# Kernel tuning notes

Measured on AMD Instinct MI355X. Metric: run time of the kernel, lower is better.

## Reference

```python
import jax, jax.numpy as jnp
import numpy as np

B = 512      # batch
T = 16       # tokens per instruction
V = 1000     # vocab
E = 4        # num_experts
K = 1        # active experts per layer
NLAYERS = 3
TOPK_LOGIC = 32


def _conv(x, w, b, stride=2):
    # x: [B,Cin,H,W], w: [Cout,Cin,3,3] (OIHW), padding=1, stride=2
    y = jax.lax.conv_general_dilated(
        x, w, window_strides=(stride, stride), padding=((1, 1), (1, 1)),
        dimension_numbers=('NCHW', 'OIHW', 'NCHW'))
    return y + b[None, :, None, None]


def _gated_conv(x, w, b, gate):
    # w: [E,Cout,Cin,3,3], b: [E,Cout], gate: [B,E] 0/1 mask
    # Faithful to original: all experts computed densely, then masked.
    outs = jax.vmap(lambda wi, bi: _conv(x, wi, bi))(w, b)  # [E,B,Cout,H',W']
    return jnp.einsum('ebchw,be->bchw', outs, gate)


def _topk_mask(logits, k):
    # 0/1 mask with ones at the top-k positions along the last axis
    _, idx = jax.lax.top_k(logits, k)
    return jnp.sum(jax.nn.one_hot(idx, logits.shape[-1], dtype=logits.dtype), axis=-2)


def setup_inputs() -> dict:
    key = jax.random.key(0)
    ks = jax.random.split(key, 16)
    def rn(k, shape, s=0.05):
        return jax.random.normal(k, shape, jnp.float32) * s
    return dict(
        img=jax.random.normal(ks[0], (B, 12, 56, 56), jnp.float32),
        text=jax.random.randint(ks[1], (B, T), 0, V),
        prev_action=jax.random.randint(ks[2], (B,), 0, 7),
        emb_table=rn(ks[3], (V, 32), 1.0),
        r_w1=rn(ks[4], (32, 64)), r_b1=jnp.zeros((64,), jnp.float32),
        r_w2=rn(ks[5], (64, NLAYERS * E)), r_b2=jnp.zeros((NLAYERS * E,), jnp.float32),
        l_w1=rn(ks[6], (32, 64)), l_b1=jnp.zeros((64,), jnp.float32),
        l_w2=rn(ks[7], (64, 256)), l_b2=jnp.zeros((256,), jnp.float32),
        c1_w=rn(ks[8], (E, 32, 12, 3, 3)), c1_b=jnp.zeros((E, 32), jnp.float32),
        c2_w=rn(ks[9], (E, 64, 32, 3, 3)), c2_b=jnp.zeros((E, 64), jnp.float32),
        c3_w=rn(ks[10], (E, 128, 64, 3, 3)), c3_b=jnp.zeros((E, 128), jnp.float32),
        act_emb=rn(ks[11], (7, 16), 1.0),
        f_w=rn(ks[12], (6272 + 32 + 16, 256)), f_b=jnp.zeros((256,), jnp.float32),
        h_w=rn(ks[13], (256, 5)), h_b=jnp.zeros((5,), jnp.float32),
    )


def reference(img, text, prev_action, emb_table, r_w1, r_b1, r_w2, r_b2,
              l_w1, l_b1, l_w2, l_b2, c1_w, c1_b, c2_w, c2_b, c3_w, c3_b,
              act_emb, f_w, f_b, h_w, h_b):
    # EmbeddingBag(mode='mean') over token dim
    lang = jnp.mean(emb_table[text], axis=1)                      # [B,32]
    # Router: MLP -> [B,3,E] logits, top-k scatter -> 0/1 mask
    rlog = (jax.nn.relu(lang @ r_w1 + r_b1) @ r_w2 + r_b2).reshape(-1, NLAYERS, E)
    masks = _topk_mask(rlog, K)                                   # [B,3,E]
    x = jax.nn.relu(_gated_conv(img, c1_w, c1_b, masks[:, 0, :])) # [B,32,28,28]
    x = jax.nn.relu(_gated_conv(x, c2_w, c2_b, masks[:, 1, :]))   # [B,64,14,14]
    x = jax.nn.relu(_gated_conv(x, c3_w, c3_b, masks[:, 2, :]))   # [B,128,7,7]
    vis = x.reshape(x.shape[0], -1)                               # [B,6272]
    act = act_emb[prev_action]                                    # [B,16]
    fused = jnp.concatenate([vis, lang, act], axis=1)             # [B,6320]
    hidden = fused @ f_w + f_b                                    # [B,256]
    logic = jax.nn.relu(lang @ l_w1 + l_b1) @ l_w2 + l_b2         # [B,256]
    lmask = _topk_mask(logic, TOPK_LOGIC)                         # [B,256]
    out = jax.nn.relu(hidden * lmask)                             # dropout is identity in eval
    logits = out @ h_w + h_b                                      # [B,5]
    return logits, rlog
```

## Files before the change

### kernel.cpp

```cpp
#include <hip/hip_runtime.h>
#include <hip/hip_bf16.h>


typedef __bf16 bf16x8 __attribute__((ext_vector_type(8)));
typedef float f32x4 __attribute__((ext_vector_type(4)));

__device__ __forceinline__ unsigned short f2bf(float f) {
  union { float f; unsigned u; } v; v.f = f;
  unsigned r = v.u + 0x7FFFu + ((v.u >> 16) & 1u);
  return (unsigned short)(r >> 16);
}

__device__ __forceinline__ int wswz(int b) { return b ^ (((b >> 7) & 3) << 4); }

__global__ __launch_bounds__(256) void prep_kernel(
    const int* __restrict__ text, const float* __restrict__ emb,
    const float* __restrict__ r_w1, const float* __restrict__ r_b1,
    const float* __restrict__ r_w2, const float* __restrict__ r_b2,
    const float* __restrict__ l_w1, const float* __restrict__ l_b1,
    const float* __restrict__ l_w2, const float* __restrict__ l_b2,
    const float* __restrict__ act_emb, const int* __restrict__ pa,
    const float* __restrict__ c1_w, const float* __restrict__ c2_w,
    const float* __restrict__ c3_w, const float* __restrict__ fw,
    float* __restrict__ rlog_out, int* __restrict__ eidx, float* __restrict__ lmask,
    unsigned short* __restrict__ tailb,
    unsigned short* __restrict__ wb1, unsigned short* __restrict__ wb2,
    unsigned short* __restrict__ wb3, unsigned short* __restrict__ fwT) {
  __shared__ __align__(16) unsigned short tl2[64][272];
  const int blk = blockIdx.x;
  const int tid = threadIdx.x;

  if (blk < 512) {
    int b = blk;
    int t = tid;
    __shared__ float lg[32];
    __shared__ float hr[64];
    __shared__ float hl[64];
    __shared__ float rl[12];
    __shared__ float lgc[256];

    if (t < 32) {
      const int* tb = text + b * 16;
      float s = 0.f;
#pragma unroll
      for (int tok = 0; tok < 16; ++tok) s += emb[tb[tok] * 32 + t];
      lg[t] = s * 0.0625f;
    }
    __syncthreads();

    if (t < 64) {
      float s1 = r_b1[t], s2 = l_b1[t];
      for (int k = 0; k < 32; ++k) {
        float lv = lg[k];
        s1 += lv * r_w1[k * 64 + t];
        s2 += lv * l_w1[k * 64 + t];
      }
      hr[t] = fmaxf(s1, 0.f);
      hl[t] = fmaxf(s2, 0.f);
    }
    if (t < 64) {
      float v = 0.f;
      if (t < 32) v = lg[t];
      else if (t < 48) v = act_emb[pa[b] * 16 + (t - 32)];
      tailb[b * 64 + t] = f2bf(v);
    }
    __syncthreads();

    if (t < 12) {
      float s = r_b2[t];
      for (int k = 0; k < 64; ++k) s += hr[k] * r_w2[k * 12 + t];
      rl[t] = s;
      rlog_out[b * 12 + t] = s;
    }
    {
      float s = l_b2[t];
      for (int k = 0; k < 64; ++k) s += hl[k] * l_w2[k * 256 + t];
      lgc[t] = s;
    }
    __syncthreads();

    if (t < 3) {
      int best = 0;
      float bv = rl[t * 4];
      for (int e = 1; e < 4; ++e) {
        float v = rl[t * 4 + e];
        if (v > bv) { bv = v; best = e; }
      }
      eidx[b * 3 + t] = best;
    }
    {
      float v = lgc[t];
      int cnt = 0;
      for (int k = 0; k < 256; ++k) {
        float u = lgc[k];
        cnt += (u > v) || (u == v && k < t);
      }
      lmask[b * 256 + t] = (cnt < 32) ? 1.f : 0.f;
    }
  } else if (blk < 2080) {
    int idx = (blk - 512) * 256 + tid;
    if (idx < 24576) {
      int k = idx % 192, ec = idx / 192;
      float v = 0.f;
      if (k < 144) {
        int g = k >> 4, ci = k & 15;
        if (ci < 12) v = c1_w[ec * 108 + ci * 9 + g];
      }
      wb1[idx] = f2bf(v);
    } else if (idx < 106496) {
      int i2 = idx - 24576;
      int k = i2 % 320, ec = i2 / 320;
      float v = 0.f;
      if (k < 288) {
        int g = k >> 5, ci = k & 31;
        v = c2_w[ec * 288 + ci * 9 + g];
      }
      wb2[i2] = f2bf(v);
    } else {
      int i3 = idx - 106496;
      int k = i3 % 576, ec = i3 / 576;
      int g = k >> 6, ci = k & 63;
      wb3[i3] = f2bf(c3_w[ec * 576 + ci * 9 + g]);
    }
  } else {
    int kb = blk - 2080;
    int k0 = kb * 64;
#pragma unroll
    for (int rg = 0; rg < 4; ++rg) {
      int rl = rg * 16 + (tid >> 4);
      int srow;
      bool valid;
      if (kb < 98) {
        srow = ((kb & 1) * 64 + rl) * 49 + (kb >> 1);
        valid = true;
      } else {
        srow = 6272 + rl;
        valid = (rl < 48);
      }
#pragma unroll
      for (int c = 0; c < 4; ++c) {
        int col = ((tid & 15) + c * 16) * 4;
        float4 v = valid ? *(const float4*)&fw[(size_t)srow * 256 + col]
                         : (float4){0.f, 0.f, 0.f, 0.f};
        tl2[rl][col + 0] = f2bf(v.x);
        tl2[rl][col + 1] = f2bf(v.y);
        tl2[rl][col + 2] = f2bf(v.z);
        tl2[rl][col + 3] = f2bf(v.w);
      }
    }
    __syncthreads();
#pragma unroll
    for (int np = 0; np < 4; ++np) {
      int n = np * 64 + (tid >> 2);
      int kc = (tid & 3) * 16;
      unsigned short vv[16];
#pragma unroll
      for (int i = 0; i < 16; ++i) vv[i] = tl2[kc + i][n];
      unsigned short* dst = fwT + (size_t)n * 6336 + k0 + kc;
      *(uint4*)dst = *(const uint4*)&vv[0];
      *(uint4*)(dst + 8) = *(const uint4*)&vv[8];
    }
  }
}

__global__ __launch_bounds__(256) void conv1_fused(
    const float* __restrict__ img, const unsigned short* __restrict__ wb,
    const float* __restrict__ bias, const int* __restrict__ eidx,
    unsigned short* __restrict__ out, int* __restrict__ cnt,
    int* __restrict__ perm) {
  __shared__ __align__(16) char win[25536];
  __shared__ __align__(16) char ldsB[3 * 4096];
  const int tid = threadIdx.x;

  if (blockIdx.x >= 3584) {
    int* el = (int*)win;
    int* cc = el + 512;
    int l = blockIdx.x - 3584;
    el[tid] = eidx[tid * 3 + l];
    el[tid + 256] = eidx[(tid + 256) * 3 + l];
    __syncthreads();
    if (tid < 4) {
      int c = 0;
      for (int b = 0; b < 512; ++b) c += (el[b] == tid);
      cc[tid] = c;
      cnt[l * 4 + tid] = c;
    }
    __syncthreads();
#pragma unroll
    for (int rep = 0; rep < 2; ++rep) {
      int b = tid + rep * 256;
      int e = el[b];
      int rank = 0;
      for (int bp = 0; bp < b; ++bp) rank += (el[bp] == e);
      int off = 0;
      for (int ee = 0; ee < e; ++ee) off += cc[ee];
      perm[l * 512 + off + rank] = b;
    }
    return;
  }

  const int xcd = blockIdx.x & 7;
  const int u = blockIdx.x >> 3;
  const int t = u % 7;
  const int s = (u / 7) * 8 + xcd;
  const int e = eidx[s * 3];
  const int lane = tid & 63;
  const int wid = tid >> 6;
  const int wm0 = wid * 32;

  const int p0 = t * 128;
  const int ohmin = p0 / 28;
  const int ih0 = ohmin * 2 - 1;

  const float* ibase = img + (size_t)s * 37632;
  float vv[9][4];
  int bp9[9];
  bool ok9[9];
#pragma unroll
  for (int it = 0; it < 9; ++it) {
    int c = tid + it * 256;
    int q = c / 728;
    int rem = c - q * 728;
    int ihl = rem / 56;
    int iw = rem - ihl * 56;
    int ih = ih0 + ihl;
    bool ok = (c < 2184) && ((unsigned)ih < 56u);
    ok9[it] = ok;
    bp9[it] = (ihl * 57 + iw + 1) * 32 + q * 8;
    if (ok) {
      const float* src = ibase + q * 12544 + ih * 56 + iw;
      vv[it][0] = src[0];
      vv[it][1] = src[3136];
      vv[it][2] = src[6272];
      vv[it][3] = src[9408];
    }
  }
  uint4 bstg[3];
  int bdst[3];
  {
    const unsigned short* wbe = wb + e * (32 * 192);
#pragma unroll
    for (int c = 0; c < 3; ++c) {
      int cc = tid + 256 * c;
      int n = cc / 24, cb = cc - n * 24;
      int kt = cb >> 3, cbl = cb & 7;
      bstg[c] = *(const uint4*)(wbe + n * 192 + cb * 8);
      bdst[c] = kt * 4096 + n * 128 + ((cbl * 16) ^ ((n & 7) << 4));
    }
  }
  __builtin_amdgcn_sched_barrier(0);

  {
    uint4 z; z.x = z.y = z.z = z.w = 0u;
    for (int i = tid; i < 1596; i += 256) ((uint4*)win)[i] = z;
  }
#pragma unroll
  for (int c = 0; c < 3; ++c) *(uint4*)(ldsB + bdst[c]) = bstg[c];
  __syncthreads();

#pragma unroll
  for (int it = 0; it < 9; ++it) {
    if (ok9[it]) {
      unsigned short w4[4] = {f2bf(vv[it][0]), f2bf(vv[it][1]),
                              f2bf(vv[it][2]), f2bf(vv[it][3])};
      *(unsigned long long*)(win + wswz(bp9[it])) = *(const unsigned long long*)w4;
    }
  }

  int ohl[2], owr[2];
#pragma unroll
  for (int mf = 0; mf < 2; ++mf) {
    int m = wm0 + mf * 16 + (lane & 15);
    int p = p0 + m;
    if (p > 783) p = 783;
    int oh = p / 28;
    owr[mf] = p - oh * 28;
    ohl[mf] = (oh - ohmin) * 2;
  }
  const int lg = lane >> 4;
  const int ci0 = (lg & 1) * 8;
  const int lgh = lg >> 1;
  int brdo[2], brx[2];
#pragma unroll
  for (int nf = 0; nf < 2; ++nf) {
    int n = nf * 16 + (lane & 15);
    brdo[nf] = n * 128;
    brx[nf] = (n & 7) << 4;
  }

  f32x4 acc[2][2];
#pragma unroll
  for (int mf = 0; mf < 2; ++mf)
#pragma unroll
    for (int nf = 0; nf < 2; ++nf) acc[mf][nf] = (f32x4){0.f, 0.f, 0.f, 0.f};

  __syncthreads();

#pragma unroll
  for (int kt = 0; kt < 3; ++kt) {
#pragma unroll
    for (int ks = 0; ks < 2; ++ks) {
      const int g = kt * 4 + ks * 2 + lgh;
      const int kh = g / 3;
      const int kw = g - kh * 3;
      const bool gv = (g < 9);
      bf16x8 af[2];
#pragma unroll
      for (int mf = 0; mf < 2; ++mf) {
        int iwp = owr[mf] * 2 + kw;
        int ihl = ohl[mf] + kh;
        int bp = gv ? ((ihl * 57 + iwp) * 32 + ci0 * 2)
                    : (13 * 57 * 32 + ci0 * 2);
        af[mf] = __builtin_bit_cast(bf16x8, *(const uint4*)(win + wswz(bp)));
      }
      bf16x8 bfv[2];
      const int cb = ks * 64 + ((lane >> 4) << 4);
#pragma unroll
      for (int nf = 0; nf < 2; ++nf)
        bfv[nf] = __builtin_bit_cast(bf16x8,
            *(const uint4*)(ldsB + kt * 4096 + brdo[nf] + (cb ^ brx[nf])));
#pragma unroll
      for (int mf = 0; mf < 2; ++mf)
#pragma unroll
        for (int nf = 0; nf < 2; ++nf)
          acc[mf][nf] = __builtin_amdgcn_mfma_f32_16x16x32_bf16(af[mf], bfv[nf], acc[mf][nf], 0, 0, 0);
    }
  }

  const int col = lane & 15;
  const int rg = (lane >> 4) * 4;
  const float b0 = bias[e * 32 + col];
  const float b1 = bias[e * 32 + 16 + col];
#pragma unroll
  for (int mf = 0; mf < 2; ++mf)
#pragma unroll
    for (int r = 0; r < 4; ++r) {
      int m = wm0 + mf * 16 + rg + r;
      int p = p0 + m;
      if (p < 784) {
        size_t ob = ((size_t)s * 784 + p) * 32;
        out[ob + col]      = f2bf(fmaxf(acc[mf][0][r] + b0, 0.f));
        out[ob + 16 + col] = f2bf(fmaxf(acc[mf][1][r] + b1, 0.f));
      }
    }
}

template<int CIN, int H, int OH, int KREAL, int KP, int COUT,
         int WGM, int WGN, int MF, int NF>
__global__ __launch_bounds__(256) void conv_mfma(
    const unsigned short* __restrict__ in, const unsigned short* __restrict__ wb,
    const float* __restrict__ bias, const int* __restrict__ cnt,
    const int* __restrict__ perm, unsigned short* __restrict__ out) {
  constexpr int PerS = OH * OH;
  constexpr int BM = WGM * MF * 16;
  constexpr int BN = WGN * NF * 16;
  constexpr int AJ = BM / 32;
  constexpr int KT = KP / 64;
  constexpr int W = H;
  constexpr int BCH = BN / 32;

  int bm = blockIdx.x;
  int e = 0, row0 = 0, rows = 0;
  bool found = false;
  {
    int acc = 0, ebase = 0;
#pragma unroll
    for (int ee = 0; ee < 4; ++ee) {
      int er = cnt[ee] * PerS;
      int te = (er + BM - 1) / BM;
      if (!found && bm < acc + te) {
        e = ee;
        row0 = ebase + (bm - acc) * BM;
        rows = er - (bm - acc) * BM;
        if (rows > BM) rows = BM;
        found = true;
      }
      acc += te;
      ebase += er;
    }
  }
  if (!found) return;

  __shared__ __align__(16) char lds[BM * 128 + BN * 128];
  char* ldsB = lds + BM * 128;
  const int tid = threadIdx.x;
  const int lane = tid & 63;
  const int wid = tid >> 6;
  const int wm0 = (wid / WGN) * (MF * 16);
  const int wn0 = (wid % WGN) * (NF * 16);
  const int c16 = tid & 7;

  int ihc[AJ], iwc[AJ], abase[AJ], adso[AJ];
#pragma unroll
  for (int j = 0; j < AJ; ++j) {
    int r = (tid >> 3) + 32 * j;
    int gr = row0 + r;
    const int MAXR = 512 * PerS - 1;
    if (gr > MAXR) gr = MAXR;
    int sord = gr / PerS;
    int p = gr - sord * PerS;
    int s = perm[sord];
    int oh = p / OH, ow = p - oh * OH;
    ihc[j] = oh * 2 - 1;
    iwc[j] = ow * 2 - 1;
    abase[j] = s * (H * W);
    adso[j] = r * 128 + ((c16 * 16) ^ ((r & 7) << 4));
  }
  const unsigned short* wbe = wb + (size_t)e * COUT * KP;
  int bgo[BCH], bdso[BCH];
#pragma unroll
  for (int c = 0; c < BCH; ++c) {
    int cc = tid + 256 * c;
    int n = cc >> 3, cb = cc & 7;
    bgo[c] = n * KP + cb * 8;
    bdso[c] = n * 128 + ((cb * 16) ^ ((n & 7) << 4));
  }
  int ardo[MF], arx[MF], brdo[NF], brx[NF];
#pragma unroll
  for (int mf = 0; mf < MF; ++mf) {
    int r = wm0 + mf * 16 + (lane & 15);
    ardo[mf] = r * 128;
    arx[mf] = (r & 7) << 4;
  }
#pragma unroll
  for (int nf = 0; nf < NF; ++nf) {
    int n = wn0 + nf * 16 + (lane & 15);
    brdo[nf] = n * 128;
    brx[nf] = (n & 7) << 4;
  }

  auto loadA = [&](int kt, int j) -> uint4 {
    uint4 z; z.x = z.y = z.z = z.w = 0u;
    int kbase = kt * 64 + c16 * 8;
    if (kbase >= KREAL) return z;
    int g = kbase / CIN;
    int ci0 = kbase - g * CIN;
    int kh = g / 3, kw = g - (g / 3) * 3;
    int ih = ihc[j] + kh, iw = iwc[j] + kw;
    if ((unsigned)ih >= (unsigned)H || (unsigned)iw >= (unsigned)W) return z;
    const unsigned short* p = in + ((size_t)(abase[j] + ih * W + iw) * CIN + ci0);
    return *(const uint4*)p;
  };

  uint4 rA[AJ], rB[BCH];
#pragma unroll
  for (int j = 0; j < AJ; ++j) rA[j] = loadA(0, j);
#pragma unroll
  for (int c = 0; c < BCH; ++c) rB[c] = *(const uint4*)(wbe + bgo[c]);

  f32x4 acc[MF][NF];
#pragma unroll
  for (int mf = 0; mf < MF; ++mf)
#pragma unroll
    for (int nf = 0; nf < NF; ++nf) acc[mf][nf] = (f32x4){0.f, 0.f, 0.f, 0.f};

  for (int kt = 0; kt < KT; ++kt) {
    __syncthreads();
#pragma unroll
    for (int j = 0; j < AJ; ++j) *(uint4*)(lds + adso[j]) = rA[j];
#pragma unroll
    for (int c = 0; c < BCH; ++c) *(uint4*)(ldsB + bdso[c]) = rB[c];
    __syncthreads();
    if (kt + 1 < KT) {
#pragma unroll
      for (int j = 0; j < AJ; ++j) rA[j] = loadA(kt + 1, j);
#pragma unroll
      for (int c = 0; c < BCH; ++c) rB[c] = *(const uint4*)(wbe + bgo[c] + (kt + 1) * 64);
    }
#pragma unroll
    for (int ks = 0; ks < 2; ++ks) {
      int cb = ks * 64 + ((lane >> 4) << 4);
      bf16x8 af[MF], bfv[NF];
#pragma unroll
      for (int mf = 0; mf < MF; ++mf)
        af[mf] = __builtin_bit_cast(bf16x8, *(const uint4*)(lds + ardo[mf] + (cb ^ arx[mf])));
#pragma unroll
      for (int nf = 0; nf < NF; ++nf)
        bfv[nf] = __builtin_bit_cast(bf16x8, *(const uint4*)(ldsB + brdo[nf] + (cb ^ brx[nf])));
#pragma unroll
      for (int mf = 0; mf < MF; ++mf)
#pragma unroll
        for (int nf = 0; nf < NF; ++nf)
          acc[mf][nf] = __builtin_amdgcn_mfma_f32_16x16x32_bf16(af[mf], bfv[nf], acc[mf][nf], 0, 0, 0);
    }
  }

  const int col = lane & 15;
  const int rg = (lane >> 4) * 4;
#pragma unroll
  for (int mf = 0; mf < MF; ++mf) {
#pragma unroll
    for (int r = 0; r < 4; ++r) {
      int m = wm0 + mf * 16 + rg + r;
      if (m < rows) {
        int gr = row0 + m;
        int sord = gr / PerS;
        int p = gr - sord * PerS;
        int s = perm[sord];
        size_t ob = ((size_t)s * PerS + p) * COUT;
#pragma unroll
        for (int nf = 0; nf < NF; ++nf) {
          int co = wn0 + nf * 16 + col;
          float v = acc[mf][nf][r] + bias[e * COUT + co];
          out[ob + co] = f2bf(fmaxf(v, 0.f));
        }
      }
    }
  }
}

__global__ __launch_bounds__(256) void fgemm_kernel(
    const unsigned short* __restrict__ x3, const unsigned short* __restrict__ tail,
    const unsigned short* __restrict__ fwT, float* __restrict__ partial) {
  constexpr int MF = 2, NF = 2;
  const int row0 = blockIdx.x * 64;
  const int nc0 = blockIdx.y * 64;
  const int kz = blockIdx.z * 704;
  __shared__ __align__(16) char lds[64 * 128 + 64 * 128];
  char* ldsB = lds + 64 * 128;
  const int tid = threadIdx.x;
  const int lane = tid & 63;
  const int wid = tid >> 6;
  const int wm0 = (wid >> 1) * 32;
  const int wn0 = (wid & 1) * 32;
  const int c16 = tid & 7;
  int arow[2], adso[2];
#pragma unroll
  for (int j = 0; j < 2; ++j) {
    int r = (tid >> 3) + 32 * j;
    arow[j] = row0 + r;
    adso[j] = r * 128 + ((c16 * 16) ^ ((r & 7) << 4));
  }
  int bgo[2], bdso[2];
#pragma unroll
  for (int c = 0; c < 2; ++c) {
    int cc = tid + 256 * c;
    int n = cc >> 3, cb = cc & 7;
    bgo[c] = (nc0 + n) * 6336 + kz + cb * 8;
    bdso[c] = n * 128 + ((cb * 16) ^ ((n & 7) << 4));
  }
  int ardo[MF], arx[MF], brdo[NF], brx[NF];
#pragma unroll
  for (int mf = 0; mf < MF; ++mf) {
    int r = wm0 + mf * 16 + (lane & 15);
    ardo[mf] = r * 128; arx[mf] = (r & 7) << 4;
  }
#pragma unroll
  for (int nf = 0; nf < NF; ++nf) {
    int n = wn0 + nf * 16 + (lane & 15);
    brdo[nf] = n * 128; brx[nf] = (n & 7) << 4;
  }
  auto loadA = [&](int kt, int j) -> uint4 {
    int k = kz + kt * 64 + c16 * 8;
    const unsigned short* p;
    if (k < 6272) p = x3 + (size_t)arow[j] * 6272 + k;
    else p = tail + arow[j] * 64 + (k - 6272);
    return *(const uint4*)p;
  };
  uint4 rA[2], rB[2];
#pragma unroll
  for (int j = 0; j < 2; ++j) rA[j] = loadA(0, j);
#pragma unroll
  for (int c = 0; c < 2; ++c) rB[c] = *(const uint4*)(fwT + bgo[c]);
  f32x4 acc[MF][NF];
#pragma unroll
  for (int mf = 0; mf < MF; ++mf)
#pragma unroll
    for (int nf = 0; nf < NF; ++nf) acc[mf][nf] = (f32x4){0.f, 0.f, 0.f, 0.f};

  for (int kt = 0; kt < 11; ++kt) {
    __syncthreads();
#pragma unroll
    for (int j = 0; j < 2; ++j) *(uint4*)(lds + adso[j]) = rA[j];
#pragma unroll
    for (int c = 0; c < 2; ++c) *(uint4*)(ldsB + bdso[c]) = rB[c];
    __syncthreads();
    if (kt + 1 < 11) {
#pragma unroll
      for (int j = 0; j < 2; ++j) rA[j] = loadA(kt + 1, j);
#pragma unroll
      for (int c = 0; c < 2; ++c) rB[c] = *(const uint4*)(fwT + bgo[c] + (kt + 1) * 64);
    }
#pragma unroll
    for (int ks = 0; ks < 2; ++ks) {
      int cb = ks * 64 + ((lane >> 4) << 4);
      bf16x8 af[MF], bfv[NF];
#pragma unroll
      for (int mf = 0; mf < MF; ++mf)
        af[mf] = __builtin_bit_cast(bf16x8, *(const uint4*)(lds + ardo[mf] + (cb ^ arx[mf])));
#pragma unroll
      for (int nf = 0; nf < NF; ++nf)
        bfv[nf] = __builtin_bit_cast(bf16x8, *(const uint4*)(ldsB + brdo[nf] + (cb ^ brx[nf])));
#pragma unroll
      for (int mf = 0; mf < MF; ++mf)
#pragma unroll
        for (int nf = 0; nf < NF; ++nf)
          acc[mf][nf] = __builtin_amdgcn_mfma_f32_16x16x32_bf16(af[mf], bfv[nf], acc[mf][nf], 0, 0, 0);
    }
  }
  const int col = lane & 15;
  const int rg = (lane >> 4) * 4;
  float* pz = partial + (size_t)blockIdx.z * 131072;
#pragma unroll
  for (int mf = 0; mf < MF; ++mf)
#pragma unroll
    for (int r = 0; r < 4; ++r) {
      int m = wm0 + mf * 16 + rg + r;
      int grow = row0 + m;
#pragma unroll
      for (int nf = 0; nf < 2; ++nf) {
        int n = nc0 + wn0 + nf * 16 + col;
        pz[grow * 256 + n] = acc[mf][nf][r];
      }
    }
}

__global__ __launch_bounds__(256) void reduce_head(const float* __restrict__ part,
                                                   const float* __restrict__ f_b,
                                                   const float* __restrict__ lmask,
                                                   const float* __restrict__ h_w,
                                                   const float* __restrict__ h_b,
                                                   float* __restrict__ logits) {
  int b = blockIdx.x, t = threadIdx.x;
  float s = f_b[t];
#pragma unroll
  for (int z = 0; z < 9; ++z) s += part[z * 131072 + b * 256 + t];
  __shared__ float o[256];
  o[t] = (lmask[b * 256 + t] != 0.f) ? fmaxf(s, 0.f) : 0.f;
  __syncthreads();
  if (t < 5) {
    float v = h_b[t];
    for (int n = 0; n < 256; ++n) v += o[n] * h_w[n * 5 + t];
    logits[b * 5 + t] = v;
  }
}

extern "C" void kernel_launch(void* const* d_in, const int* in_sizes, int n_in,
                              void* d_out, int out_size, void* d_ws, size_t ws_size,
                              hipStream_t stream) {
  (void)in_sizes; (void)n_in; (void)out_size; (void)ws_size;
  const float* img       = (const float*)d_in[0];
  const int*   text      = (const int*)d_in[1];
  const int*   pa        = (const int*)d_in[2];
  const float* emb_table = (const float*)d_in[3];
  const float* r_w1 = (const float*)d_in[4];
  const float* r_b1 = (const float*)d_in[5];
  const float* r_w2 = (const float*)d_in[6];
  const float* r_b2 = (const float*)d_in[7];
  const float* l_w1 = (const float*)d_in[8];
  const float* l_b1 = (const float*)d_in[9];
  const float* l_w2 = (const float*)d_in[10];
  const float* l_b2 = (const float*)d_in[11];
  const float* c1_w = (const float*)d_in[12];
  const float* c1_b = (const float*)d_in[13];
  const float* c2_w = (const float*)d_in[14];
  const float* c2_b = (const float*)d_in[15];
  const float* c3_w = (const float*)d_in[16];
  const float* c3_b = (const float*)d_in[17];
  const float* act_emb = (const float*)d_in[18];
  const float* f_w = (const float*)d_in[19];
  const float* f_b = (const float*)d_in[20];
  const float* h_w = (const float*)d_in[21];
  const float* h_b = (const float*)d_in[22];

  float* outf   = (float*)d_out;
  float* logits = outf;
  float* rlog   = outf + 2560;

  char* cur = (char*)d_ws;
  auto alloc = [&](size_t bytes) { char* r = cur; cur += (bytes + 255) & ~(size_t)255; return r; };
  float* lmask   = (float*)alloc(131072 * 4);
  int* eidx      = (int*)alloc(1536 * 4);
  int* cnt       = (int*)alloc(12 * 4);
  int* perm      = (int*)alloc(1536 * 4);
  unsigned short* wb1  = (unsigned short*)alloc((size_t)24576 * 2);
  unsigned short* wb2  = (unsigned short*)alloc((size_t)81920 * 2);
  unsigned short* wb3  = (unsigned short*)alloc((size_t)294912 * 2);
  unsigned short* fwT  = (unsigned short*)alloc((size_t)1622016 * 2);
  unsigned short* tailb= (unsigned short*)alloc((size_t)32768 * 2);
  unsigned short* x1b  = (unsigned short*)alloc((size_t)12845056 * 2);
  unsigned short* x2b  = (unsigned short*)alloc((size_t)6422528 * 2);
  unsigned short* x3b  = (unsigned short*)alloc((size_t)3211264 * 2);
  float* partial       = (float*)alloc((size_t)9 * 131072 * 4);

  prep_kernel<<<2179, 256, 0, stream>>>(text, emb_table,
                                        r_w1, r_b1, r_w2, r_b2,
                                        l_w1, l_b1, l_w2, l_b2,
                                        act_emb, pa,
                                        c1_w, c2_w, c3_w, f_w,
                                        rlog, eidx, lmask, tailb,
                                        wb1, wb2, wb3, fwT);

  conv1_fused<<<3587, 256, 0, stream>>>(img, wb1, c1_b, eidx, x1b, cnt, perm);
  conv_mfma<32, 28, 14, 288, 320, 64, 2, 2, 4, 2>
      <<<787, 256, 0, stream>>>(x1b, wb2, c2_b, cnt + 4, perm + 512, x2b);
  conv_mfma<64, 14, 7, 576, 576, 128, 1, 4, 4, 2>
      <<<395, 256, 0, stream>>>(x2b, wb3, c3_b, cnt + 8, perm + 1024, x3b);

  fgemm_kernel<<<dim3(8, 4, 9), 256, 0, stream>>>(x3b, tailb, fwT, partial);
  reduce_head<<<512, 256, 0, stream>>>(partial, f_b, lmask, h_w, h_b, logits);
}
```

Baseline: 138.3 us.

## Fuse prep and conv1 into one kernel with per-block router recompute

Merges the prep kernel and the conv1 kernel into a single launch. Each conv1 block recomputes its sample's layer-0 router expert from the text embedding and converts its expert's conv1 weights to bf16 in place, instead of reading precomputed eidx and wb1. The three perm blocks recompute the router for all samples on their own. This removes one kernel launch and the serial dependency between them, at the cost of redundant router MLP and weight-conversion work in every conv1 block plus heavier per-thread router loops in the perm blocks.

```diff
diff --git a/kernel.cpp b/kernel.cpp
--- a/kernel.cpp
+++ b/kernel.cpp
@@ -13,7 +13,8 @@
 
 __device__ __forceinline__ int wswz(int b) { return b ^ (((b >> 7) & 3) << 4); }
 
-__global__ __launch_bounds__(256) void prep_kernel(
+__global__ __launch_bounds__(256) void megaA(
+    const float* __restrict__ img,
     const int* __restrict__ text, const float* __restrict__ emb,
     const float* __restrict__ r_w1, const float* __restrict__ r_b1,
     const float* __restrict__ r_w2, const float* __restrict__ r_b2,
@@ -22,22 +23,265 @@
     const float* __restrict__ act_emb, const int* __restrict__ pa,
     const float* __restrict__ c1_w, const float* __restrict__ c2_w,
     const float* __restrict__ c3_w, const float* __restrict__ fw,
-    float* __restrict__ rlog_out, int* __restrict__ eidx, float* __restrict__ lmask,
+    const float* __restrict__ c1_b,
+    float* __restrict__ rlog_out, float* __restrict__ lmask,
     unsigned short* __restrict__ tailb,
-    unsigned short* __restrict__ wb1, unsigned short* __restrict__ wb2,
-    unsigned short* __restrict__ wb3, unsigned short* __restrict__ fwT) {
-  __shared__ __align__(16) unsigned short tl2[64][272];
+    unsigned short* __restrict__ wb2, unsigned short* __restrict__ wb3,
+    unsigned short* __restrict__ fwT,
+    unsigned short* __restrict__ x1b,
+    int* __restrict__ cnt, int* __restrict__ perm) {
+  __shared__ __align__(16) char shm[38400];
+  const int tid = threadIdx.x;
   const int blk = blockIdx.x;
-  const int tid = threadIdx.x;
-
-  if (blk < 512) {
-    int b = blk;
+
+  if (blk < 3584) {
+    char* win  = shm;
+    char* ldsB = shm + 25536;
+    float* shLang = (float*)(shm + 37888);
+    float* shHr   = shLang + 32;
+    float* shRl   = shHr + 64;
+
+    const int xcd = blk & 7;
+    const int u = blk >> 3;
+    const int t = u % 7;
+    const int s = (u / 7) * 8 + xcd;
+    const int lane = tid & 63;
+    const int wid = tid >> 6;
+    const int wm0 = wid * 32;
+
+    const int p0 = t * 128;
+    const int ohmin = p0 / 28;
+    const int ih0 = ohmin * 2 - 1;
+
+    const float* ibase = img + (size_t)s * 37632;
+    float vv[9][4];
+    int bp9[9];
+    bool ok9[9];
+#pragma unroll
+    for (int it = 0; it < 9; ++it) {
+      int c = tid + it * 256;
+      int q = c / 728;
+      int rem = c - q * 728;
+      int ihl = rem / 56;
+      int iw = rem - ihl * 56;
+      int ih = ih0 + ihl;
+      bool ok = (c < 2184) && ((unsigned)ih < 56u);
+      ok9[it] = ok;
+      bp9[it] = (ihl * 57 + iw + 1) * 32 + q * 8;
+      if (ok) {
+        const float* src = ibase + q * 12544 + ih * 56 + iw;
+        vv[it][0] = src[0];
+        vv[it][1] = src[3136];
+        vv[it][2] = src[6272];
+        vv[it][3] = src[9408];
+      }
+    }
+    __builtin_amdgcn_sched_barrier(0);
+
+    if (tid < 32) {
+      const int* tb = text + s * 16;
+      float acc = 0.f;
+#pragma unroll
+      for (int tok = 0; tok < 16; ++tok) acc += emb[tb[tok] * 32 + tid];
+      shLang[tid] = acc * 0.0625f;
+    }
+    __syncthreads();
+    if (tid < 64) {
+      float s1 = r_b1[tid];
+      for (int k = 0; k < 32; ++k) s1 += shLang[k] * r_w1[k * 64 + tid];
+      shHr[tid] = fmaxf(s1, 0.f);
+    }
+    __syncthreads();
+    if (tid < 4) {
+      float v = r_b2[tid];
+      for (int k = 0; k < 64; ++k) v += shHr[k] * r_w2[k * 12 + tid];
+      shRl[tid] = v;
+    }
+    __syncthreads();
+    int e;
+    {
+      float r0 = shRl[0], r1 = shRl[1], r2 = shRl[2], r3 = shRl[3];
+      int best = 0; float bv = r0;
+      if (r1 > bv) { bv = r1; best = 1; }
+      if (r2 > bv) { bv = r2; best = 2; }
+      if (r3 > bv) { bv = r3; best = 3; }
+      e = best;
+    }
+
+    unsigned short w8s[3][8];
+    int bdst[3];
+    {
+      const float* c1e = c1_w + e * 3456;
+#pragma unroll
+      for (int c = 0; c < 3; ++c) {
+        int cc = tid + 256 * c;
+        int n = cc / 24, cb = cc - n * 24;
+#pragma unroll
+        for (int j = 0; j < 8; ++j) {
+          int k = cb * 8 + j;
+          int g = k >> 4, ci = k & 15;
+          float v = (g < 9 && ci < 12) ? c1e[n * 108 + ci * 9 + g] : 0.f;
+          w8s[c][j] = f2bf(v);
+        }
+        int kt = cb >> 3, cbl = cb & 7;
+        bdst[c] = kt * 4096 + n * 128 + ((cbl * 16) ^ ((n & 7) << 4));
+      }
+    }
+    {
+      uint4 z; z.x = z.y = z.z = z.w = 0u;
+      for (int i = tid; i < 1596; i += 256) ((uint4*)win)[i] = z;
+    }
+#pragma unroll
+    for (int c = 0; c < 3; ++c) *(uint4*)(ldsB + bdst[c]) = *(const uint4*)w8s[c];
+    __syncthreads();
+
+#pragma unroll
+    for (int it = 0; it < 9; ++it) {
+      if (ok9[it]) {
+        unsigned short w4[4] = {f2bf(vv[it][0]), f2bf(vv[it][1]),
+                                f2bf(vv[it][2]), f2bf(vv[it][3])};
+        *(unsigned long long*)(win + wswz(bp9[it])) = *(const unsigned long long*)w4;
+      }
+    }
+
+    int ohl[2], owr[2];
+#pragma unroll
+    for (int mf = 0; mf < 2; ++mf) {
+      int m = wm0 + mf * 16 + (lane & 15);
+      int p = p0 + m;
+      if (p > 783) p = 783;
+      int oh = p / 28;
+      owr[mf] = p - oh * 28;
+      ohl[mf] = (oh - ohmin) * 2;
+    }
+    const int lg = lane >> 4;
+    const int ci0 = (lg & 1) * 8;
+    const int lgh = lg >> 1;
+    int brdo[2], brx[2];
+#pragma unroll
+    for (int nf = 0; nf < 2; ++nf) {
+      int n = nf * 16 + (lane & 15);
+      brdo[nf] = n * 128;
+      brx[nf] = (n & 7) << 4;
+    }
+
+    f32x4 acc[2][2];
+#pragma unroll
+    for (int mf = 0; mf < 2; ++mf)
+#pragma unroll
+      for (int nf = 0; nf < 2; ++nf) acc[mf][nf] = (f32x4){0.f, 0.f, 0.f, 0.f};
+
+    __syncthreads();
+
+#pragma unroll
+    for (int kt = 0; kt < 3; ++kt) {
+#pragma unroll
+      for (int ks = 0; ks < 2; ++ks) {
+        const int g = kt * 4 + ks * 2 + lgh;
+        const int kh = g / 3;
+        const int kw = g - kh * 3;
+        const bool gv = (g < 9);
+        bf16x8 af[2];
+#pragma unroll
+        for (int mf = 0; mf < 2; ++mf) {
+          int iwp = owr[mf] * 2 + kw;
+          int ihl = ohl[mf] + kh;
+          int bp = gv ? ((ihl * 57 + iwp) * 32 + ci0 * 2)
+                      : (13 * 57 * 32 + ci0 * 2);
+          af[mf] = __builtin_bit_cast(bf16x8, *(const uint4*)(win + wswz(bp)));
+        }
+        bf16x8 bfv[2];
+        const int cb = ks * 64 + ((lane >> 4) << 4);
+#pragma unroll
+        for (int nf = 0; nf < 2; ++nf)
+          bfv[nf] = __builtin_bit_cast(bf16x8,
+              *(const uint4*)(ldsB + kt * 4096 + brdo[nf] + (cb ^ brx[nf])));
+#pragma unroll
+        for (int mf = 0; mf < 2; ++mf)
+#pragma unroll
+          for (int nf = 0; nf < 2; ++nf)
+            acc[mf][nf] = __builtin_amdgcn_mfma_f32_16x16x32_bf16(af[mf], bfv[nf], acc[mf][nf], 0, 0, 0);
+      }
+    }
+
+    const int col = lane & 15;
+    const int rg = (lane >> 4) * 4;
+    const float b0 = c1_b[e * 32 + col];
+    const float b1 = c1_b[e * 32 + 16 + col];
+#pragma unroll
+    for (int mf = 0; mf < 2; ++mf)
+#pragma unroll
+      for (int r = 0; r < 4; ++r) {
+        int m = wm0 + mf * 16 + rg + r;
+        int p = p0 + m;
+        if (p < 784) {
+          size_t ob = ((size_t)s * 784 + p) * 32;
+          x1b[ob + col]      = f2bf(fmaxf(acc[mf][0][r] + b0, 0.f));
+          x1b[ob + 16 + col] = f2bf(fmaxf(acc[mf][1][r] + b1, 0.f));
+        }
+      }
+  } else if (blk < 3587) {
+    int* el = (int*)shm;
+    int* ccx = el + 512;
+    int l = blk - 3584;
+#pragma unroll
+    for (int rep = 0; rep < 2; ++rep) {
+      int b = tid + rep * 256;
+      const int* tb = text + b * 16;
+      float lang[32];
+#pragma unroll
+      for (int d = 0; d < 32; ++d) lang[d] = 0.f;
+#pragma unroll
+      for (int tok = 0; tok < 16; ++tok) {
+        int row = tb[tok] * 32;
+#pragma unroll
+        for (int d = 0; d < 32; ++d) lang[d] += emb[row + d];
+      }
+#pragma unroll
+      for (int d = 0; d < 32; ++d) lang[d] *= 0.0625f;
+      float rl4[4];
+#pragma unroll
+      for (int tt = 0; tt < 4; ++tt) rl4[tt] = r_b2[l * 4 + tt];
+#pragma unroll 2
+      for (int k = 0; k < 64; ++k) {
+        float hk = r_b1[k];
+#pragma unroll
+        for (int j = 0; j < 32; ++j) hk += lang[j] * r_w1[j * 64 + k];
+        hk = fmaxf(hk, 0.f);
+#pragma unroll
+        for (int tt = 0; tt < 4; ++tt) rl4[tt] += hk * r_w2[k * 12 + l * 4 + tt];
+      }
+      int best = 0; float bv = rl4[0];
+#pragma unroll
+      for (int ee = 1; ee < 4; ++ee) { if (rl4[ee] > bv) { bv = rl4[ee]; best = ee; } }
+      el[b] = best;
+    }
+    __syncthreads();
+    if (tid < 4) {
+      int c = 0;
+      for (int b = 0; b < 512; ++b) c += (el[b] == tid);
+      ccx[tid] = c;
+      cnt[l * 4 + tid] = c;
+    }
+    __syncthreads();
+#pragma unroll
+    for (int rep = 0; rep < 2; ++rep) {
+      int b = tid + rep * 256;
+      int e = el[b];
+      int rank = 0;
+      for (int bp = 0; bp < b; ++bp) rank += (el[bp] == e);
+      int off = 0;
+      for (int ee = 0; ee < e; ++ee) off += ccx[ee];
+      perm[l * 512 + off + rank] = b;
+    }
+  } else if (blk < 4099) {
+    int b = blk - 3587;
     int t = tid;
-    __shared__ float lg[32];
-    __shared__ float hr[64];
-    __shared__ float hl[64];
-    __shared__ float rl[12];
-    __shared__ float lgc[256];
+    float* lg   = (float*)shm;
+    float* hr   = lg + 32;
+    float* hl   = hr + 64;
+    float* rl   = hl + 64;
+    float* lgc  = rl + 12;
 
     if (t < 32) {
       const int* tb = text + b * 16;
@@ -79,51 +323,34 @@
     }
     __syncthreads();
 
-    if (t < 3) {
-      int best = 0;
-      float bv = rl[t * 4];
-      for (int e = 1; e < 4; ++e) {
-        float v = rl[t * 4 + e];
-        if (v > bv) { bv = v; best = e; }
-      }
-      eidx[b * 3 + t] = best;
-    }
     {
       float v = lgc[t];
-      int cnt = 0;
+      int cnt2 = 0;
       for (int k = 0; k < 256; ++k) {
-        float u = lgc[k];
-        cnt += (u > v) || (u == v && k < t);
-      }
-      lmask[b * 256 + t] = (cnt < 32) ? 1.f : 0.f;
-    }
-  } else if (blk < 2080) {
-    int idx = (blk - 512) * 256 + tid;
-    if (idx < 24576) {
-      int k = idx % 192, ec = idx / 192;
-      float v = 0.f;
-      if (k < 144) {
-        int g = k >> 4, ci = k & 15;
-        if (ci < 12) v = c1_w[ec * 108 + ci * 9 + g];
-      }
-      wb1[idx] = f2bf(v);
-    } else if (idx < 106496) {
-      int i2 = idx - 24576;
-      int k = i2 % 320, ec = i2 / 320;
+        float u2 = lgc[k];
+        cnt2 += (u2 > v) || (u2 == v && k < t);
+      }
+      lmask[b * 256 + t] = (cnt2 < 32) ? 1.f : 0.f;
+    }
+  } else if (blk < 5571) {
+    int idx = (blk - 4099) * 256 + tid;
+    if (idx < 81920) {
+      int k = idx % 320, ec = idx / 320;
       float v = 0.f;
       if (k < 288) {
         int g = k >> 5, ci = k & 31;
         v = c2_w[ec * 288 + ci * 9 + g];
       }
-      wb2[i2] = f2bf(v);
+      wb2[idx] = f2bf(v);
     } else {
-      int i3 = idx - 106496;
+      int i3 = idx - 81920;
       int k = i3 % 576, ec = i3 / 576;
       int g = k >> 6, ci = k & 63;
       wb3[i3] = f2bf(c3_w[ec * 576 + ci * 9 + g]);
     }
   } else {
-    int kb = blk - 2080;
+    unsigned short(*tl2)[272] = (unsigned short(*)[272])shm;
+    int kb = blk - 5571;
     int k0 = kb * 64;
 #pragma unroll
     for (int rg = 0; rg < 4; ++rg) {
@@ -153,196 +380,14 @@
     for (int np = 0; np < 4; ++np) {
       int n = np * 64 + (tid >> 2);
       int kc = (tid & 3) * 16;
-      unsigned short vv[16];
-#pragma unroll
-      for (int i = 0; i < 16; ++i) vv[i] = tl2[kc + i][n];
+      unsigned short vv2[16];
+#pragma unroll
+      for (int i = 0; i < 16; ++i) vv2[i] = tl2[kc + i][n];
       unsigned short* dst = fwT + (size_t)n * 6336 + k0 + kc;
-      *(uint4*)dst = *(const uint4*)&vv[0];
-      *(uint4*)(dst + 8) = *(const uint4*)&vv[8];
-    }
-  }
-}
-
-__global__ __launch_bounds__(256) void conv1_fused(
-    const float* __restrict__ img, const unsigned short* __restrict__ wb,
-    const float* __restrict__ bias, const int* __restrict__ eidx,
-    unsigned short* __restrict__ out, int* __restrict__ cnt,
-    int* __restrict__ perm) {
-  __shared__ __align__(16) char win[25536];
-  __shared__ __align__(16) char ldsB[3 * 4096];
-  const int tid = threadIdx.x;
-
-  if (blockIdx.x >= 3584) {
-    int* el = (int*)win;
-    int* cc = el + 512;
-    int l = blockIdx.x - 3584;
-    el[tid] = eidx[tid * 3 + l];
-    el[tid + 256] = eidx[(tid + 256) * 3 + l];
-    __syncthreads();
-    if (tid < 4) {
-      int c = 0;
-      for (int b = 0; b < 512; ++b) c += (el[b] == tid);
-      cc[tid] = c;
-      cnt[l * 4 + tid] = c;
-    }
-    __syncthreads();
-#pragma unroll
-    for (int rep = 0; rep < 2; ++rep) {
-      int b = tid + rep * 256;
-      int e = el[b];
-      int rank = 0;
-      for (int bp = 0; bp < b; ++bp) rank += (el[bp] == e);
-      int off = 0;
-      for (int ee = 0; ee < e; ++ee) off += cc[ee];
-      perm[l * 512 + off + rank] = b;
-    }
-    return;
-  }
-
-  const int xcd = blockIdx.x & 7;
-  const int u = blockIdx.x >> 3;
-  const int t = u % 7;
-  const int s = (u / 7) * 8 + xcd;
-  const int e = eidx[s * 3];
-  const int lane = tid & 63;
-  const int wid = tid >> 6;
-  const int wm0 = wid * 32;
-
-  const int p0 = t * 128;
-  const int ohmin = p0 / 28;
-  const int ih0 = ohmin * 2 - 1;
-
-  const float* ibase = img + (size_t)s * 37632;
-  float vv[9][4];
-  int bp9[9];
-  bool ok9[9];
-#pragma unroll
-  for (int it = 0; it < 9; ++it) {
-    int c = tid + it * 256;
-    int q = c / 728;
-    int rem = c - q * 728;
-    int ihl = rem / 56;
-    int iw = rem - ihl * 56;
-    int ih = ih0 + ihl;
-    bool ok = (c < 2184) && ((unsigned)ih < 56u);
-    ok9[it] = ok;
-    bp9[it] = (ihl * 57 + iw + 1) * 32 + q * 8;
-    if (ok) {
-      const float* src = ibase + q * 12544 + ih * 56 + iw;
-      vv[it][0] = src[0];
-      vv[it][1] = src[3136];
-      vv[it][2] = src[6272];
-      vv[it][3] = src[9408];
-    }
-  }
-  uint4 bstg[3];
-  int bdst[3];
-  {
-    const unsigned short* wbe = wb + e * (32 * 192);
-#pragma unroll
-    for (int c = 0; c < 3; ++c) {
-      int cc = tid + 256 * c;
-      int n = cc / 24, cb = cc - n * 24;
-      int kt = cb >> 3, cbl = cb & 7;
-      bstg[c] = *(const uint4*)(wbe + n * 192 + cb * 8);
-      bdst[c] = kt * 4096 + n * 128 + ((cbl * 16) ^ ((n & 7) << 4));
-    }
-  }
-  __builtin_amdgcn_sched_barrier(0);
-
-  {
-    uint4 z; z.x = z.y = z.z = z.w = 0u;
-    for (int i = tid; i < 1596; i += 256) ((uint4*)win)[i] = z;
-  }
-#pragma unroll
-  for (int c = 0; c < 3; ++c) *(uint4*)(ldsB + bdst[c]) = bstg[c];
-  __syncthreads();
-
-#pragma unroll
-  for (int it = 0; it < 9; ++it) {
-    if (ok9[it]) {
-      unsigned short w4[4] = {f2bf(vv[it][0]), f2bf(vv[it][1]),
-                              f2bf(vv[it][2]), f2bf(vv[it][3])};
-      *(unsigned long long*)(win + wswz(bp9[it])) = *(const unsigned long long*)w4;
-    }
-  }
-
-  int ohl[2], owr[2];
-#pragma unroll
-  for (int mf = 0; mf < 2; ++mf) {
-    int m = wm0 + mf * 16 + (lane & 15);
-    int p = p0 + m;
-    if (p > 783) p = 783;
-    int oh = p / 28;
-    owr[mf] = p - oh * 28;
-    ohl[mf] = (oh - ohmin) * 2;
-  }
-  const int lg = lane >> 4;
-  const int ci0 = (lg & 1) * 8;
-  const int lgh = lg >> 1;
-  int brdo[2], brx[2];
-#pragma unroll
-  for (int nf = 0; nf < 2; ++nf) {
-    int n = nf * 16 + (lane & 15);
-    brdo[nf] = n * 128;
-    brx[nf] = (n & 7) << 4;
-  }
-
-  f32x4 acc[2][2];
-#pragma unroll
-  for (int mf = 0; mf < 2; ++mf)
-#pragma unroll
-    for (int nf = 0; nf < 2; ++nf) acc[mf][nf] = (f32x4){0.f, 0.f, 0.f, 0.f};
-
-  __syncthreads();
-
-#pragma unroll
-  for (int kt = 0; kt < 3; ++kt) {
-#pragma unroll
-    for (int ks = 0; ks < 2; ++ks) {
-      const int g = kt * 4 + ks * 2 + lgh;
-      const int kh = g / 3;
-      const int kw = g - kh * 3;
-      const bool gv = (g < 9);
-      bf16x8 af[2];
-#pragma unroll
-      for (int mf = 0; mf < 2; ++mf) {
-        int iwp = owr[mf] * 2 + kw;
-        int ihl = ohl[mf] + kh;
-        int bp = gv ? ((ihl * 57 + iwp) * 32 + ci0 * 2)
-                    : (13 * 57 * 32 + ci0 * 2);
-        af[mf] = __builtin_bit_cast(bf16x8, *(const uint4*)(win + wswz(bp)));
-      }
-      bf16x8 bfv[2];
-      const int cb = ks * 64 + ((lane >> 4) << 4);
-#pragma unroll
-      for (int nf = 0; nf < 2; ++nf)
-        bfv[nf] = __builtin_bit_cast(bf16x8,
-            *(const uint4*)(ldsB + kt * 4096 + brdo[nf] + (cb ^ brx[nf])));
-#pragma unroll
-      for (int mf = 0; mf < 2; ++mf)
-#pragma unroll
-        for (int nf = 0; nf < 2; ++nf)
-          acc[mf][nf] = __builtin_amdgcn_mfma_f32_16x16x32_bf16(af[mf], bfv[nf], acc[mf][nf], 0, 0, 0);
-    }
-  }
-
-  const int col = lane & 15;
-  const int rg = (lane >> 4) * 4;
-  const float b0 = bias[e * 32 + col];
-  const float b1 = bias[e * 32 + 16 + col];
-#pragma unroll
-  for (int mf = 0; mf < 2; ++mf)
-#pragma unroll
-    for (int r = 0; r < 4; ++r) {
-      int m = wm0 + mf * 16 + rg + r;
-      int p = p0 + m;
-      if (p < 784) {
-        size_t ob = ((size_t)s * 784 + p) * 32;
-        out[ob + col]      = f2bf(fmaxf(acc[mf][0][r] + b0, 0.f));
-        out[ob + 16 + col] = f2bf(fmaxf(acc[mf][1][r] + b1, 0.f));
-      }
-    }
+      *(uint4*)dst = *(const uint4*)&vv2[0];
+      *(uint4*)(dst + 8) = *(const uint4*)&vv2[8];
+    }
+  }
 }
 
 template<int CIN, int H, int OH, int KREAL, int KP, int COUT,
@@ -670,10 +715,8 @@
   char* cur = (char*)d_ws;
   auto alloc = [&](size_t bytes) { char* r = cur; cur += (bytes + 255) & ~(size_t)255; return r; };
   float* lmask   = (float*)alloc(131072 * 4);
-  int* eidx      = (int*)alloc(1536 * 4);
   int* cnt       = (int*)alloc(12 * 4);
   int* perm      = (int*)alloc(1536 * 4);
-  unsigned short* wb1  = (unsigned short*)alloc((size_t)24576 * 2);
   unsigned short* wb2  = (unsigned short*)alloc((size_t)81920 * 2);
   unsigned short* wb3  = (unsigned short*)alloc((size_t)294912 * 2);
   unsigned short* fwT  = (unsigned short*)alloc((size_t)1622016 * 2);
@@ -683,15 +726,14 @@
   unsigned short* x3b  = (unsigned short*)alloc((size_t)3211264 * 2);
   float* partial       = (float*)alloc((size_t)9 * 131072 * 4);
 
-  prep_kernel<<<2179, 256, 0, stream>>>(text, emb_table,
-                                        r_w1, r_b1, r_w2, r_b2,
-                                        l_w1, l_b1, l_w2, l_b2,
-                                        act_emb, pa,
-                                        c1_w, c2_w, c3_w, f_w,
-                                        rlog, eidx, lmask, tailb,
-                                        wb1, wb2, wb3, fwT);
-
-  conv1_fused<<<3587, 256, 0, stream>>>(img, wb1, c1_b, eidx, x1b, cnt, perm);
+  megaA<<<5670, 256, 0, stream>>>(img, text, emb_table,
+                                  r_w1, r_b1, r_w2, r_b2,
+                                  l_w1, l_b1, l_w2, l_b2,
+                                  act_emb, pa,
+                                  c1_w, c2_w, c3_w, f_w, c1_b,
+                                  rlog, lmask, tailb,
+                                  wb2, wb3, fwT, x1b, cnt, perm);
+
   conv_mfma<32, 28, 14, 288, 320, 64, 2, 2, 4, 2>
       <<<787, 256, 0, stream>>>(x1b, wb2, c2_b, cnt + 4, perm + 512, x2b);
   conv_mfma<64, 14, 7, 576, 576, 128, 1, 4, 4, 2>
```

Measured after the change: 212.9 us. 1.54x slower.

## Move weight conversion into conv1 kernel and build conv1 weights inline

Applied to the files above, without the earlier changes.

The conv2/conv3 weight bf16 repacking and the fc weight transpose move out of the prep kernel into extra blocks of the conv1 kernel, so they run alongside conv1 instead of lengthening the serial prep stage. Conv1 blocks now read fp32 c1 weights directly and convert them to bf16 in registers, which removes the intermediate wb1 buffer and its dependency on prep. The cost is more scalar global loads per conv1 block and a larger combined shared-memory footprint.

```diff
diff --git a/kernel.cpp b/kernel.cpp
--- a/kernel.cpp
+++ b/kernel.cpp
@@ -20,157 +20,150 @@
     const float* __restrict__ l_w1, const float* __restrict__ l_b1,
     const float* __restrict__ l_w2, const float* __restrict__ l_b2,
     const float* __restrict__ act_emb, const int* __restrict__ pa,
-    const float* __restrict__ c1_w, const float* __restrict__ c2_w,
-    const float* __restrict__ c3_w, const float* __restrict__ fw,
     float* __restrict__ rlog_out, int* __restrict__ eidx, float* __restrict__ lmask,
-    unsigned short* __restrict__ tailb,
-    unsigned short* __restrict__ wb1, unsigned short* __restrict__ wb2,
-    unsigned short* __restrict__ wb3, unsigned short* __restrict__ fwT) {
-  __shared__ __align__(16) unsigned short tl2[64][272];
-  const int blk = blockIdx.x;
-  const int tid = threadIdx.x;
-
-  if (blk < 512) {
-    int b = blk;
-    int t = tid;
-    __shared__ float lg[32];
-    __shared__ float hr[64];
-    __shared__ float hl[64];
-    __shared__ float rl[12];
-    __shared__ float lgc[256];
-
-    if (t < 32) {
-      const int* tb = text + b * 16;
-      float s = 0.f;
-#pragma unroll
-      for (int tok = 0; tok < 16; ++tok) s += emb[tb[tok] * 32 + t];
-      lg[t] = s * 0.0625f;
-    }
-    __syncthreads();
-
-    if (t < 64) {
-      float s1 = r_b1[t], s2 = l_b1[t];
-      for (int k = 0; k < 32; ++k) {
-        float lv = lg[k];
-        s1 += lv * r_w1[k * 64 + t];
-        s2 += lv * l_w1[k * 64 + t];
-      }
-      hr[t] = fmaxf(s1, 0.f);
-      hl[t] = fmaxf(s2, 0.f);
-    }
-    if (t < 64) {
-      float v = 0.f;
-      if (t < 32) v = lg[t];
-      else if (t < 48) v = act_emb[pa[b] * 16 + (t - 32)];
-      tailb[b * 64 + t] = f2bf(v);
-    }
-    __syncthreads();
-
-    if (t < 12) {
-      float s = r_b2[t];
-      for (int k = 0; k < 64; ++k) s += hr[k] * r_w2[k * 12 + t];
-      rl[t] = s;
-      rlog_out[b * 12 + t] = s;
-    }
-    {
-      float s = l_b2[t];
-      for (int k = 0; k < 64; ++k) s += hl[k] * l_w2[k * 256 + t];
-      lgc[t] = s;
-    }
-    __syncthreads();
-
-    if (t < 3) {
-      int best = 0;
-      float bv = rl[t * 4];
-      for (int e = 1; e < 4; ++e) {
-        float v = rl[t * 4 + e];
-        if (v > bv) { bv = v; best = e; }
-      }
-      eidx[b * 3 + t] = best;
-    }
-    {
-      float v = lgc[t];
-      int cnt = 0;
-      for (int k = 0; k < 256; ++k) {
-        float u = lgc[k];
-        cnt += (u > v) || (u == v && k < t);
-      }
-      lmask[b * 256 + t] = (cnt < 32) ? 1.f : 0.f;
-    }
-  } else if (blk < 2080) {
-    int idx = (blk - 512) * 256 + tid;
-    if (idx < 24576) {
-      int k = idx % 192, ec = idx / 192;
-      float v = 0.f;
-      if (k < 144) {
-        int g = k >> 4, ci = k & 15;
-        if (ci < 12) v = c1_w[ec * 108 + ci * 9 + g];
-      }
-      wb1[idx] = f2bf(v);
-    } else if (idx < 106496) {
-      int i2 = idx - 24576;
-      int k = i2 % 320, ec = i2 / 320;
-      float v = 0.f;
-      if (k < 288) {
-        int g = k >> 5, ci = k & 31;
-        v = c2_w[ec * 288 + ci * 9 + g];
-      }
-      wb2[i2] = f2bf(v);
-    } else {
-      int i3 = idx - 106496;
-      int k = i3 % 576, ec = i3 / 576;
-      int g = k >> 6, ci = k & 63;
-      wb3[i3] = f2bf(c3_w[ec * 576 + ci * 9 + g]);
-    }
-  } else {
-    int kb = blk - 2080;
-    int k0 = kb * 64;
-#pragma unroll
-    for (int rg = 0; rg < 4; ++rg) {
-      int rl = rg * 16 + (tid >> 4);
-      int srow;
-      bool valid;
-      if (kb < 98) {
-        srow = ((kb & 1) * 64 + rl) * 49 + (kb >> 1);
-        valid = true;
-      } else {
-        srow = 6272 + rl;
-        valid = (rl < 48);
-      }
-#pragma unroll
-      for (int c = 0; c < 4; ++c) {
-        int col = ((tid & 15) + c * 16) * 4;
-        float4 v = valid ? *(const float4*)&fw[(size_t)srow * 256 + col]
-                         : (float4){0.f, 0.f, 0.f, 0.f};
-        tl2[rl][col + 0] = f2bf(v.x);
-        tl2[rl][col + 1] = f2bf(v.y);
-        tl2[rl][col + 2] = f2bf(v.z);
-        tl2[rl][col + 3] = f2bf(v.w);
-      }
-    }
-    __syncthreads();
-#pragma unroll
-    for (int np = 0; np < 4; ++np) {
-      int n = np * 64 + (tid >> 2);
-      int kc = (tid & 3) * 16;
-      unsigned short vv[16];
-#pragma unroll
-      for (int i = 0; i < 16; ++i) vv[i] = tl2[kc + i][n];
-      unsigned short* dst = fwT + (size_t)n * 6336 + k0 + kc;
-      *(uint4*)dst = *(const uint4*)&vv[0];
-      *(uint4*)(dst + 8) = *(const uint4*)&vv[8];
-    }
+    unsigned short* __restrict__ tailb) {
+  int b = blockIdx.x;
+  int t = threadIdx.x;
+  __shared__ float lg[32];
+  __shared__ float hr[64];
+  __shared__ float hl[64];
+  __shared__ float rl[12];
+  __shared__ float lgc[256];
+
+  if (t < 32) {
+    const int* tb = text + b * 16;
+    float s = 0.f;
+#pragma unroll
+    for (int tok = 0; tok < 16; ++tok) s += emb[tb[tok] * 32 + t];
+    lg[t] = s * 0.0625f;
+  }
+  __syncthreads();
+
+  if (t < 64) {
+    float s1 = r_b1[t], s2 = l_b1[t];
+    for (int k = 0; k < 32; ++k) {
+      float lv = lg[k];
+      s1 += lv * r_w1[k * 64 + t];
+      s2 += lv * l_w1[k * 64 + t];
+    }
+    hr[t] = fmaxf(s1, 0.f);
+    hl[t] = fmaxf(s2, 0.f);
+  }
+  if (t < 64) {
+    float v = 0.f;
+    if (t < 32) v = lg[t];
+    else if (t < 48) v = act_emb[pa[b] * 16 + (t - 32)];
+    tailb[b * 64 + t] = f2bf(v);
+  }
+  __syncthreads();
+
+  if (t < 12) {
+    float s = r_b2[t];
+    for (int k = 0; k < 64; ++k) s += hr[k] * r_w2[k * 12 + t];
+    rl[t] = s;
+    rlog_out[b * 12 + t] = s;
+  }
+  {
+    float s = l_b2[t];
+    for (int k = 0; k < 64; ++k) s += hl[k] * l_w2[k * 256 + t];
+    lgc[t] = s;
+  }
+  __syncthreads();
+
+  if (t < 3) {
+    int best = 0;
+    float bv = rl[t * 4];
+    for (int e = 1; e < 4; ++e) {
+      float v = rl[t * 4 + e];
+      if (v > bv) { bv = v; best = e; }
+    }
+    eidx[b * 3 + t] = best;
+  }
+  {
+    float v = lgc[t];
+    int cnt = 0;
+    for (int k = 0; k < 256; ++k) {
+      float u = lgc[k];
+      cnt += (u > v) || (u == v && k < t);
+    }
+    lmask[b * 256 + t] = (cnt < 32) ? 1.f : 0.f;
   }
 }
 
 __global__ __launch_bounds__(256) void conv1_fused(
-    const float* __restrict__ img, const unsigned short* __restrict__ wb,
+    const float* __restrict__ img, const float* __restrict__ c1_w,
     const float* __restrict__ bias, const int* __restrict__ eidx,
     unsigned short* __restrict__ out, int* __restrict__ cnt,
-    int* __restrict__ perm) {
-  __shared__ __align__(16) char win[25536];
-  __shared__ __align__(16) char ldsB[3 * 4096];
+    int* __restrict__ perm,
+    const float* __restrict__ c2_w, const float* __restrict__ c3_w,
+    const float* __restrict__ fw,
+    unsigned short* __restrict__ wb1,
+    unsigned short* __restrict__ wb2, unsigned short* __restrict__ wb3,
+    unsigned short* __restrict__ fwT) {
+  __shared__ __align__(16) char shm[38400];
+  char* win  = shm;
+  char* ldsB = shm + 25536;
   const int tid = threadIdx.x;
+
+  if (blockIdx.x >= 3587) {
+    if (blockIdx.x < 5059) {
+      int idx = (blockIdx.x - 3587) * 256 + tid;
+      if (idx < 81920) {
+        int k = idx % 320, ec = idx / 320;
+        float v = 0.f;
+        if (k < 288) {
+          int g = k >> 5, ci = k & 31;
+          v = c2_w[ec * 288 + ci * 9 + g];
+        }
+        wb2[idx] = f2bf(v);
+      } else {
+        int i3 = idx - 81920;
+        int k = i3 % 576, ec = i3 / 576;
+        int g = k >> 6, ci = k & 63;
+        wb3[i3] = f2bf(c3_w[ec * 576 + ci * 9 + g]);
+      }
+    } else {
+      unsigned short(*tl2)[272] = (unsigned short(*)[272])shm;
+      int kb = blockIdx.x - 5059;
+      int k0 = kb * 64;
+#pragma unroll
+      for (int rg = 0; rg < 4; ++rg) {
+        int rl = rg * 16 + (tid >> 4);
+        int srow;
+        bool valid;
+        if (kb < 98) {
+          srow = ((kb & 1) * 64 + rl) * 49 + (kb >> 1);
+          valid = true;
+        } else {
+          srow = 6272 + rl;
+          valid = (rl < 48);
+        }
+#pragma unroll
+        for (int c = 0; c < 4; ++c) {
+          int col = ((tid & 15) + c * 16) * 4;
+          float4 v = valid ? *(const float4*)&fw[(size_t)srow * 256 + col]
+                           : (float4){0.f, 0.f, 0.f, 0.f};
+          tl2[rl][col + 0] = f2bf(v.x);
+          tl2[rl][col + 1] = f2bf(v.y);
+          tl2[rl][col + 2] = f2bf(v.z);
+          tl2[rl][col + 3] = f2bf(v.w);
+        }
+      }
+      __syncthreads();
+#pragma unroll
+      for (int np = 0; np < 4; ++np) {
+        int n = np * 64 + (tid >> 2);
+        int kc = (tid & 3) * 16;
+        unsigned short vv2[16];
+#pragma unroll
+        for (int i = 0; i < 16; ++i) vv2[i] = tl2[kc + i][n];
+        unsigned short* dst = fwT + (size_t)n * 6336 + k0 + kc;
+        *(uint4*)dst = *(const uint4*)&vv2[0];
+        *(uint4*)(dst + 8) = *(const uint4*)&vv2[8];
+      }
+    }
+    return;
+  }
 
   if (blockIdx.x >= 3584) {
     int* el = (int*)win;
@@ -235,19 +228,26 @@
       vv[it][3] = src[9408];
     }
   }
-  uint4 bstg[3];
+  unsigned short w8s[3][8];
   int bdst[3];
   {
-    const unsigned short* wbe = wb + e * (32 * 192);
+    const float* c1e = c1_w + e * 3456;
 #pragma unroll
     for (int c = 0; c < 3; ++c) {
       int cc = tid + 256 * c;
       int n = cc / 24, cb = cc - n * 24;
+#pragma unroll
+      for (int j = 0; j < 8; ++j) {
+        int k = cb * 8 + j;
+        int g = k >> 4, ci = k & 15;
+        float v = (g < 9 && ci < 12) ? c1e[n * 108 + ci * 9 + g] : 0.f;
+        w8s[c][j] = f2bf(v);
+      }
       int kt = cb >> 3, cbl = cb & 7;
-      bstg[c] = *(const uint4*)(wbe + n * 192 + cb * 8);
       bdst[c] = kt * 4096 + n * 128 + ((cbl * 16) ^ ((n & 7) << 4));
     }
   }
+  (void)wb1;
   __builtin_amdgcn_sched_barrier(0);
 
   {
@@ -255,7 +255,7 @@
     for (int i = tid; i < 1596; i += 256) ((uint4*)win)[i] = z;
   }
 #pragma unroll
-  for (int c = 0; c < 3; ++c) *(uint4*)(ldsB + bdst[c]) = bstg[c];
+  for (int c = 0; c < 3; ++c) *(uint4*)(ldsB + bdst[c]) = *(const uint4*)w8s[c];
   __syncthreads();
 
 #pragma unroll
@@ -683,15 +683,14 @@
   unsigned short* x3b  = (unsigned short*)alloc((size_t)3211264 * 2);
   float* partial       = (float*)alloc((size_t)9 * 131072 * 4);
 
-  prep_kernel<<<2179, 256, 0, stream>>>(text, emb_table,
-                                        r_w1, r_b1, r_w2, r_b2,
-                                        l_w1, l_b1, l_w2, l_b2,
-                                        act_emb, pa,
-                                        c1_w, c2_w, c3_w, f_w,
-                                        rlog, eidx, lmask, tailb,
-                                        wb1, wb2, wb3, fwT);
-
-  conv1_fused<<<3587, 256, 0, stream>>>(img, wb1, c1_b, eidx, x1b, cnt, perm);
+  prep_kernel<<<512, 256, 0, stream>>>(text, emb_table,
+                                       r_w1, r_b1, r_w2, r_b2,
+                                       l_w1, l_b1, l_w2, l_b2,
+                                       act_emb, pa,
+                                       rlog, eidx, lmask, tailb);
+
+  conv1_fused<<<5158, 256, 0, stream>>>(img, c1_w, c1_b, eidx, x1b, cnt, perm,
+                                        c2_w, c3_w, f_w, wb1, wb2, wb3, fwT);
   conv_mfma<32, 28, 14, 288, 320, 64, 2, 2, 4, 2>
       <<<787, 256, 0, stream>>>(x1b, wb2, c2_b, cnt + 4, perm + 512, x2b);
   conv_mfma<64, 14, 7, 576, 576, 128, 1, 4, 4, 2>
```

Result: no change. 141.0 us (+1.9%).
